# Performance work log

Measured on AMD Instinct MI355X. Metric: run time of the kernel, lower is better.

Reference implementation:

```python
import jax, jax.numpy as jnp
import numpy as np

_ELECTRODE_POSITIONS = jnp.array([[0.3, 0.25, 0.0], [-0.3, 0.25, 0.0], [-0.05, -0.4, 0.0],
                                  [0.03, 0.05, 0.2], [0.0, 0.05, 0.22], [-0.04, 0.01, 0.21],
                                  [-0.08, -0.02, 0.18], [-0.14, -0.02, 0.13], [-0.2, -0.02, 0.07]],
                                 dtype=jnp.float32)

B, N, T, K, H = 8, 1024, 512, 9, 32


def setup_inputs() -> dict:
    key = jax.random.key(0)
    ks = jax.random.split(key, 9)
    d = jax.random.normal(ks[1], (B, N, 3), jnp.float32)
    d = d / jnp.linalg.norm(d, axis=-1, keepdims=True)  # unit dipole directions
    return {
        'position': jax.random.normal(ks[0], (B, N, 3), jnp.float32) * 0.1,
        'dipole_dir': d,
        'amplitude': jax.random.uniform(ks[2], (B, N), jnp.float32),
        'envelope_t': jax.random.normal(ks[3], (B, N, T), jnp.float32),
        'electrode_offset': jax.random.normal(ks[4], (B, K, 3), jnp.float32) * 0.01,
        'W1': jax.random.normal(ks[5], (H, 7), jnp.float32) * 0.3,
        'b1': jax.random.normal(ks[6], (H,), jnp.float32) * 0.1,
        'W2': jax.random.normal(ks[7], (1, H), jnp.float32) * 0.3,
        'b2': jax.random.normal(ks[8], (1,), jnp.float32) * 0.1,
    }


def _attenuation(position, E, W1, b1, W2, b2):
    # position [B,N,3], E [B,K,3] -> correction [B,N,K]
    pos_exp = jnp.broadcast_to(position[:, :, None, :], (B, N, K, 3))
    r_vec = E[:, None, :, :] - position[:, :, None, :]          # [B,N,K,3]
    r_dist = jnp.maximum(jnp.linalg.norm(r_vec, axis=-1, keepdims=True), 1e-6)
    r_hat = r_vec / r_dist
    feat = jnp.concatenate([pos_exp, r_hat, r_dist], axis=-1)   # [B,N,K,7]
    h = jax.nn.gelu(jnp.einsum('bnkf,hf->bnkh', feat, W1) + b1, approximate=False)
    raw = (jnp.einsum('bnkh,oh->bnko', h, W2) + b2)[..., 0]     # [B,N,K]
    return 1.0 + jnp.tanh(raw) * 0.5


def reference(position, dipole_dir, amplitude, envelope_t, electrode_offset, W1, b1, W2, b2):
    E = _ELECTRODE_POSITIONS[None] + electrode_offset            # [B,K,3]
    amp_env = (amplitude[..., None] * envelope_t)[:, :, None, :]  # [B,N,1,T]
    moment = dipole_dir[..., None] * amp_env                     # [B,N,3,T]
    r_vec = E[:, None, :, :] - position[:, :, None, :]           # [B,N,K,3]
    EPS_SQ = 0.04
    r_dist_sq = jnp.sum(r_vec ** 2, axis=-1)                     # [B,N,K]
    atten_denom = (r_dist_sq + EPS_SQ) ** 1.5
    correction = _attenuation(position, E, W1, b1, W2, b2)       # [B,N,K]
    dot = jnp.einsum('bndt,bnkd->bnkt', moment, r_vec)           # [B,N,K,T]
    V_per_gaussian = dot * (correction / atten_denom)[..., None]
    V_electrodes = jnp.clip(jnp.sum(V_per_gaussian, axis=1), -50.0, 50.0)  # [B,K,T]
    V_RA, V_LA, V_LL = V_electrodes[:, 0], V_electrodes[:, 1], V_electrodes[:, 2]
    V_chest = V_electrodes[:, 3:9]
    WCT = (V_RA + V_LA + V_LL) / 3.0
    leads = jnp.stack([V_LA - V_RA, V_LL - V_RA, V_LL - V_LA,
                       -(V_LA + V_LL) / 2.0 + V_RA,
                       V_LA - (V_RA + V_LL) / 2.0,
                       V_LL - (V_RA + V_LA) / 2.0], axis=1)
    chest_leads = V_chest - WCT[:, None, :]
    v_leads = jnp.concatenate([leads, chest_leads], axis=1)      # [B,12,T]
    return v_leads, V_electrodes
```

## Files before the change

kernel.cpp:

```cpp
#include <hip/hip_runtime.h>
#include <hip/hip_bf16.h>
#include <math.h>

#define BB 8
#define NN 1024
#define TT 512
#define KK 9
#define HH 32

#define NCHUNK 32
#define NPER   (NN/NCHUNK)

__constant__ float c_epos[KK][3] = {
    { 0.30f,  0.25f, 0.00f},
    {-0.30f,  0.25f, 0.00f},
    {-0.05f, -0.40f, 0.00f},
    { 0.03f,  0.05f, 0.20f},
    { 0.00f,  0.05f, 0.22f},
    {-0.04f,  0.01f, 0.21f},
    {-0.08f, -0.02f, 0.18f},
    {-0.14f, -0.02f, 0.13f},
    {-0.20f, -0.02f, 0.07f},
};

__global__ __launch_bounds__(512) void fused_kernel(
    const float* __restrict__ pos,
    const float* __restrict__ dd,
    const float* __restrict__ amp,
    const float* __restrict__ env,
    const float* __restrict__ eoff,
    const float* __restrict__ W1,
    const float* __restrict__ pb1,
    const float* __restrict__ W2,
    const float* __restrict__ pb2,
    float* __restrict__ partial)
{
    const int tid   = threadIdx.x;
    const int chunk = blockIdx.x;
    const int b     = blockIdx.y;
    const int n0    = chunk * NPER;
    const int ng    = tid >> 8;
    const int tp    = tid & 255;

    __shared__ float sW1[HH * 7];
    __shared__ float sb1[HH];
    __shared__ float sW2[HH];
    __shared__ float sb2;
    __shared__ float sE[KK][3];
    __shared__ float sA[NPER][12];
    __shared__ float2 sP[2][KK][256];

    if (tid < HH * 7) sW1[tid] = W1[tid];
    if (tid < HH)     { sb1[tid] = pb1[tid]; sW2[tid] = W2[tid]; }
    if (tid < KK * 3) sE[tid / 3][tid % 3] = c_epos[tid / 3][tid % 3] + eoff[b * KK * 3 + tid];
    if (tid == 0)     sb2 = pb2[0];

    const float2* envp = (const float2*)(env + ((size_t)(b * NN + n0 + ng * 16)) * TT) + tp;
    float2 pf[8];
    #pragma unroll
    for (int i = 0; i < 8; ++i) pf[i] = envp[(size_t)i * (TT / 2)];

    __syncthreads();

    if (tid < NPER * KK) {
        const int k  = tid % KK;
        const int nl = tid / KK;
        const int bn = b * NN + n0 + nl;

        const float px = pos[bn * 3 + 0];
        const float py = pos[bn * 3 + 1];
        const float pz = pos[bn * 3 + 2];

        const float rx = sE[k][0] - px, ry = sE[k][1] - py, rz = sE[k][2] - pz;
        const float r2 = rx * rx + ry * ry + rz * rz;
        const float d0 = r2 + 0.04f;
        const float denom = d0 * sqrtf(d0);

        const float rdist = fmaxf(sqrtf(r2), 1e-6f);
        const float rinv  = 1.0f / rdist;
        float feat[7];
        feat[0] = px; feat[1] = py; feat[2] = pz;
        feat[3] = rx * rinv; feat[4] = ry * rinv; feat[5] = rz * rinv;
        feat[6] = rdist;

        float raw = sb2;
        #pragma unroll
        for (int j = 0; j < HH; ++j) {
            float s = sb1[j];
            #pragma unroll
            for (int f = 0; f < 7; ++f) s += sW1[j * 7 + f] * feat[f];
            const float g = 0.5f * s * (1.0f + erff(s * 0.70710678118654752f));
            raw += sW2[j] * g;
        }
        const float corr = 1.0f + 0.5f * tanhf(raw);

        const float ddx = dd[bn * 3 + 0], ddy = dd[bn * 3 + 1], ddz = dd[bn * 3 + 2];
        const float dot = ddx * rx + ddy * ry + ddz * rz;

        sA[nl][k] = amp[bn] * dot * corr / denom;
    }
    __syncthreads();

    float2 acc[KK];
    #pragma unroll
    for (int k = 0; k < KK; ++k) { acc[k].x = 0.0f; acc[k].y = 0.0f; }

    const float4* s4 = (const float4*)sA;
    #pragma unroll
    for (int i = 0; i < 16; ++i) {
        const int nl = ng * 16 + i;
        const float2 ev = (i < 8) ? pf[i] : envp[(size_t)i * (TT / 2)];
        const float4 a0 = s4[nl * 3 + 0];
        const float4 a1 = s4[nl * 3 + 1];
        const float  a8 = sA[nl][8];
        acc[0].x += a0.x * ev.x; acc[0].y += a0.x * ev.y;
        acc[1].x += a0.y * ev.x; acc[1].y += a0.y * ev.y;
        acc[2].x += a0.z * ev.x; acc[2].y += a0.z * ev.y;
        acc[3].x += a0.w * ev.x; acc[3].y += a0.w * ev.y;
        acc[4].x += a1.x * ev.x; acc[4].y += a1.x * ev.y;
        acc[5].x += a1.y * ev.x; acc[5].y += a1.y * ev.y;
        acc[6].x += a1.z * ev.x; acc[6].y += a1.z * ev.y;
        acc[7].x += a1.w * ev.x; acc[7].y += a1.w * ev.y;
        acc[8].x += a8   * ev.x; acc[8].y += a8   * ev.y;
    }

    #pragma unroll
    for (int k = 0; k < KK; ++k) sP[ng][k][tp] = acc[k];
    __syncthreads();

    if (tid < 256) {
        float2* pp = (float2*)(partial + (((size_t)chunk * BB + b) * KK) * TT) + tp;
        #pragma unroll
        for (int k = 0; k < KK; ++k) {
            const float2 u = sP[0][k][tp];
            const float2 v = sP[1][k][tp];
            float2 w; w.x = u.x + v.x; w.y = u.y + v.y;
            pp[(size_t)k * (TT / 2)] = w;
        }
    }
}

__global__ __launch_bounds__(256) void finalize_kernel(
    const float* __restrict__ partial,
    float* __restrict__ out)
{
    const int tid = threadIdx.x;
    const int tl4 = tid & 7;
    const int cg  = tid >> 3;
    const int tc  = blockIdx.x;
    const int b   = blockIdx.y;
    const int t0  = tc * 32;

    float4 s[KK];
    {
        const float* base = partial + (((size_t)cg * BB + b) * KK) * TT + t0 + tl4 * 4;
        #pragma unroll
        for (int k = 0; k < KK; ++k)
            s[k] = *(const float4*)(base + (size_t)k * TT);
    }

    __shared__ float4 sV[32][KK][8];
    __shared__ float  sRf[KK][32];
    #pragma unroll
    for (int k = 0; k < KK; ++k) sV[cg][k][tl4] = s[k];
    __syncthreads();

    if (tid < KK * 8) {
        const int k  = tid >> 3;
        const int tl = tid & 7;
        float4 v = make_float4(0.f, 0.f, 0.f, 0.f);
        #pragma unroll
        for (int g = 0; g < 32; ++g) {
            const float4 u = sV[g][k][tl];
            v.x += u.x; v.y += u.y; v.z += u.z; v.w += u.w;
        }
        sRf[k][tl * 4 + 0] = fminf(fmaxf(v.x, -50.0f), 50.0f);
        sRf[k][tl * 4 + 1] = fminf(fmaxf(v.y, -50.0f), 50.0f);
        sRf[k][tl * 4 + 2] = fminf(fmaxf(v.z, -50.0f), 50.0f);
        sRf[k][tl * 4 + 3] = fminf(fmaxf(v.w, -50.0f), 50.0f);
    }
    __syncthreads();

    if (tid < 32) {
        const int t = t0 + tid;
        float V[KK];
        #pragma unroll
        for (int k = 0; k < KK; ++k) V[k] = sRf[k][tid];

        float* vleads = out;
        float* velec  = out + (size_t)BB * 12 * TT;

        #pragma unroll
        for (int k = 0; k < KK; ++k)
            velec[((size_t)b * KK + k) * TT + t] = V[k];

        const float RA = V[0], LA = V[1], LL = V[2];
        const float WCT = (RA + LA + LL) * (1.0f / 3.0f);

        float L[12];
        L[0] = LA - RA;
        L[1] = LL - RA;
        L[2] = LL - LA;
        L[3] = RA - 0.5f * (LA + LL);
        L[4] = LA - 0.5f * (RA + LL);
        L[5] = LL - 0.5f * (RA + LA);
        L[6]  = V[3] - WCT;
        L[7]  = V[4] - WCT;
        L[8]  = V[5] - WCT;
        L[9]  = V[6] - WCT;
        L[10] = V[7] - WCT;
        L[11] = V[8] - WCT;

        #pragma unroll
        for (int l = 0; l < 12; ++l)
            vleads[((size_t)b * 12 + l) * TT + t] = L[l];
    }
}

extern "C" void kernel_launch(void* const* d_in, const int* in_sizes, int n_in,
                              void* d_out, int out_size, void* d_ws, size_t ws_size,
                              hipStream_t stream) {
    const float* pos  = (const float*)d_in[0];
    const float* dd   = (const float*)d_in[1];
    const float* amp  = (const float*)d_in[2];
    const float* env  = (const float*)d_in[3];
    const float* eoff = (const float*)d_in[4];
    const float* W1   = (const float*)d_in[5];
    const float* b1   = (const float*)d_in[6];
    const float* W2   = (const float*)d_in[7];
    const float* b2   = (const float*)d_in[8];
    float* out = (float*)d_out;

    float* partial = (float*)d_ws;

    {
        dim3 grid(NCHUNK, BB);
        fused_kernel<<<grid, 512, 0, stream>>>(
            pos, dd, amp, env, eoff, W1, b1, W2, b2, partial);
    }
    {
        dim3 grid(16, BB);
        finalize_kernel<<<grid, 256, 0, stream>>>(partial, out);
    }
}
```

Measured before the change: 18.62 us.

## Fuse finalize into main kernel via per-batch atomic counter and spin-wait

Replaces the separate finalize launch with an in-kernel cross-block handoff. Each block bumps a per-batch atomic counter after writing its partials, and the first 16 blocks per batch spin until all 32 chunks have arrived, then reduce and write the leads. This removes one kernel launch and its gap, but adds a memset launch, spin-wait latency and extra shared memory per block. It relies on all 256 blocks being co-resident to avoid deadlock.

```diff
diff --git a/kernel.cpp b/kernel.cpp
--- a/kernel.cpp
+++ b/kernel.cpp
@@ -10,6 +10,8 @@
 
 #define NCHUNK 32
 #define NPER   (NN/NCHUNK)
+
+#define PARTIAL_FLOATS ((size_t)NCHUNK * BB * KK * TT)
 
 __constant__ float c_epos[KK][3] = {
     { 0.30f,  0.25f, 0.00f},
@@ -33,7 +35,9 @@
     const float* __restrict__ pb1,
     const float* __restrict__ W2,
     const float* __restrict__ pb2,
-    float* __restrict__ partial)
+    float* __restrict__ partial,
+    unsigned int* __restrict__ counter,
+    float* __restrict__ out)
 {
     const int tid   = threadIdx.x;
     const int chunk = blockIdx.x;
@@ -49,6 +53,8 @@
     __shared__ float sE[KK][3];
     __shared__ float sA[NPER][12];
     __shared__ float2 sP[2][KK][256];
+    __shared__ float4 sV[NCHUNK][KK][8];
+    __shared__ float  sRf[KK][32];
 
     if (tid < HH * 7) sW1[tid] = W1[tid];
     if (tid < HH)     { sb1[tid] = pb1[tid]; sW2[tid] = W2[tid]; }
@@ -138,31 +144,39 @@
             pp[(size_t)k * (TT / 2)] = w;
         }
     }
-}
-
-__global__ __launch_bounds__(256) void finalize_kernel(
-    const float* __restrict__ partial,
-    float* __restrict__ out)
-{
-    const int tid = threadIdx.x;
+    __syncthreads();
+
+    if (tid == 0) {
+        __threadfence();
+        __hip_atomic_fetch_add(&counter[b], 1u, __ATOMIC_RELEASE,
+                               __HIP_MEMORY_SCOPE_AGENT);
+    }
+
+    if (chunk >= 16) return;
+
+    if (tid == 0) {
+        unsigned int v;
+        long long guard = 0;
+        do {
+            v = __hip_atomic_load(&counter[b], __ATOMIC_ACQUIRE,
+                                  __HIP_MEMORY_SCOPE_AGENT);
+            if (++guard > (1LL << 30)) break;
+            __builtin_amdgcn_s_sleep(4);
+        } while (v < (unsigned int)NCHUNK);
+    }
+    __syncthreads();
+    __threadfence();
+
+    const int t0  = chunk * 32;
     const int tl4 = tid & 7;
     const int cg  = tid >> 3;
-    const int tc  = blockIdx.x;
-    const int b   = blockIdx.y;
-    const int t0  = tc * 32;
-
-    float4 s[KK];
-    {
+
+    if (tid < 256) {
         const float* base = partial + (((size_t)cg * BB + b) * KK) * TT + t0 + tl4 * 4;
         #pragma unroll
         for (int k = 0; k < KK; ++k)
-            s[k] = *(const float4*)(base + (size_t)k * TT);
-    }
-
-    __shared__ float4 sV[32][KK][8];
-    __shared__ float  sRf[KK][32];
-    #pragma unroll
-    for (int k = 0; k < KK; ++k) sV[cg][k][tl4] = s[k];
+            sV[cg][k][tl4] = *(const float4*)(base + (size_t)k * TT);
+    }
     __syncthreads();
 
     if (tid < KK * 8) {
@@ -170,7 +184,7 @@
         const int tl = tid & 7;
         float4 v = make_float4(0.f, 0.f, 0.f, 0.f);
         #pragma unroll
-        for (int g = 0; g < 32; ++g) {
+        for (int g = 0; g < NCHUNK; ++g) {
             const float4 u = sV[g][k][tl];
             v.x += u.x; v.y += u.y; v.z += u.z; v.w += u.w;
         }
@@ -231,15 +245,12 @@
     const float* b2   = (const float*)d_in[8];
     float* out = (float*)d_out;
 
-    float* partial = (float*)d_ws;
-
-    {
-        dim3 grid(NCHUNK, BB);
-        fused_kernel<<<grid, 512, 0, stream>>>(
-            pos, dd, amp, env, eoff, W1, b1, W2, b2, partial);
-    }
-    {
-        dim3 grid(16, BB);
-        finalize_kernel<<<grid, 256, 0, stream>>>(partial, out);
-    }
+    float*        partial = (float*)d_ws;
+    unsigned int* counter = (unsigned int*)((char*)d_ws + PARTIAL_FLOATS * sizeof(float));
+
+    hipMemsetAsync(counter, 0, BB * sizeof(unsigned int), stream);
+
+    dim3 grid(NCHUNK, BB);
+    fused_kernel<<<grid, 512, 0, stream>>>(
+        pos, dd, amp, env, eoff, W1, b1, W2, b2, partial, counter, out);
 }
```

After: 58.75 us. +215.6%, slower.
